# Kernel optimization log

Hardware: AMD Instinct MI355X
Metric: run time of the kernel (lower is better)

Reference implementation:

```python
import jax, jax.numpy as jnp
import numpy as np

B, N, D, H, DH = 2, 4096, 256, 8, 64   # batch, nodes, dim, heads, dim_head
INNER = H * DH
POLY_K = 3  # polynomial order -> coeffs [H, POLY_K+1]
LN_EPS = 1e-5


def setup_inputs() -> dict:
    key = jax.random.key(0)
    ks = jax.random.split(key, 8)
    s = 0.02
    return {
        "x": jax.random.normal(ks[0], (B, N, D), dtype=jnp.float32),
        "Wq": jax.random.normal(ks[1], (D, INNER), dtype=jnp.float32) * s,
        "Wk": jax.random.normal(ks[2], (D, INNER), dtype=jnp.float32) * s,
        "Wv": jax.random.normal(ks[3], (D, INNER), dtype=jnp.float32) * s,
        "Wo": jax.random.normal(ks[4], (INNER, D), dtype=jnp.float32) * s,
        "gamma": jnp.ones((DH,), dtype=jnp.float32),
        "beta": jnp.zeros((DH,), dtype=jnp.float32),
        "coeffs": jax.random.normal(ks[5], (H, POLY_K + 1), dtype=jnp.float32) * 0.5,
    }


def reference(x, Wq, Wk, Wv, Wo, gamma, beta, coeffs):
    b, n, d = x.shape
    h, dh = coeffs.shape[0], gamma.shape[0]
    # --- graph estimator: per-head softmax adjacency A = softmax(QK^T/sqrt(dh)) ---
    q = (x @ Wq).reshape(b, n, h, dh).transpose(0, 2, 1, 3)  # bhnd
    k = (x @ Wk).reshape(b, n, h, dh).transpose(0, 2, 1, 3)  # bhnd
    scale = jax.lax.rsqrt(jnp.asarray(dh, x.dtype))
    A = jax.nn.softmax(jnp.einsum('bhnd,bhmd->bhnm', q, k) * scale, axis=-1)
    # --- value projection + per-head LayerNorm over dim_head ---
    v = (x @ Wv).reshape(b, n, h, dh)
    mu = v.mean(axis=-1, keepdims=True)
    var = ((v - mu) ** 2).mean(axis=-1, keepdims=True)
    v = (v - mu) * jax.lax.rsqrt(var + LN_EPS) * gamma + beta
    v = v.transpose(0, 2, 1, 3)  # bhnd
    # --- polynomial graph filter: y = sum_k c[h,k] * A^k v ---
    y = coeffs[None, :, 0, None, None] * v
    t = v
    for kk in range(1, coeffs.shape[1]):
        t = jnp.einsum('bhnm,bhmd->bhnd', A, t)
        y = y + coeffs[None, :, kk, None, None] * t
    # --- merge heads + output projection ---
    merged = y.transpose(0, 2, 1, 3).reshape(b, n, h * dh)
    return merged @ Wo
```

## Files before the change

kernel.cpp:

```cpp
#include <hip/hip_runtime.h>
#include <stdint.h>

#define B_ 2
#define N_ 4096
#define D_ 256
#define H_ 8
#define DH_ 64
#define INNER_ 512
#define NBH 16
#define PAD 72
#define FPAD 80

typedef unsigned short ushort_t;
typedef __attribute__((ext_vector_type(8))) short short8;
typedef __attribute__((ext_vector_type(4))) float float4v;
typedef __attribute__((ext_vector_type(4))) unsigned short ushort4v;
typedef __attribute__((ext_vector_type(4))) unsigned int uint4v;

__device__ __forceinline__ ushort_t f2bf(float f) {
    union { float f; unsigned int u; } v; v.f = f;
    unsigned int r = v.u + 0x7FFFu + ((v.u >> 16) & 1u);
    return (ushort_t)(r >> 16);
}
__device__ __forceinline__ float bf2f(ushort_t u) {
    union { unsigned int u; float f; } v; v.u = ((unsigned int)u) << 16;
    return v.f;
}
__device__ __forceinline__ unsigned char f2fp8s(float f) {
    union { float f; unsigned int u; } v; v.f = f;
    unsigned int s = (v.u >> 24) & 0x80u;
    v.u &= 0x7FFFFFFFu;
    float a = v.f;
    if (a >= 448.f) return (unsigned char)(s | 0x7E);
    if (a < 0.015625f) {
        int m = (int)(a * 512.f + 0.5f);
        return (unsigned char)(s | (unsigned)m);
    }
    unsigned int u = v.u + 0x7FFFFu + ((v.u >> 20) & 1u);
    return (unsigned char)(s | (((u >> 20) & 0x7FF) - 960));
}
__device__ __forceinline__ float fexp2(float x) {
    float r;
    asm volatile("v_exp_f32 %0, %1\n\ts_nop 0" : "=v"(r) : "v"(x));
    return r;
}

__global__ __launch_bounds__(256) void prep_kernel(
    const float* __restrict__ x, const float* __restrict__ Wq,
    const float* __restrict__ Wk, const float* __restrict__ Wv,
    const float* __restrict__ Wo,
    ushort_t* __restrict__ xb, ushort_t* __restrict__ WqkvT,
    ushort_t* __restrict__ WoT) {
    int idx = blockIdx.x * 256 + threadIdx.x;
    const int total_x = B_ * N_ * D_;
    const int total_wqkv = 3 * INNER_ * D_;
    const int total_wo = D_ * INNER_;
    if (idx < total_x) { xb[idx] = f2bf(x[idx]); return; }
    idx -= total_x;
    if (idx < total_wqkv) {
        int n = idx >> 8, k = idx & 255;
        int which = n >> 9, nn = n & 511;
        const float* W = (which == 0) ? Wq : ((which == 1) ? Wk : Wv);
        WqkvT[idx] = f2bf(W[k * INNER_ + nn]);
        return;
    }
    idx -= total_wqkv;
    if (idx < total_wo) {
        int c = idx >> 9, k = idx & 511;
        WoT[idx] = f2bf(Wo[k * D_ + c]);
    }
}

__global__ __launch_bounds__(256) void proj_gemm(
    const ushort_t* __restrict__ xb, const ushort_t* __restrict__ WqkvT,
    ushort_t* __restrict__ Qb, ushort_t* __restrict__ Kb,
    ushort_t* __restrict__ Vb) {
    __shared__ ushort_t As[128][PAD];
    __shared__ ushort_t Bs[128][PAD];
    int bid = blockIdx.x;
    int tileN = bid % 12, tileM = bid / 12;
    int tid = threadIdx.x;
    int w = tid >> 6, lane = tid & 63, q = lane >> 4, r = lane & 15;
    int wr = (w & 1) * 64, wc = (w >> 1) * 64;
    float4v acc[4][4];
    for (int i = 0; i < 4; i++)
        for (int j = 0; j < 4; j++)
            for (int e = 0; e < 4; e++) acc[i][j][e] = 0.f;

    for (int k0 = 0; k0 < 256; k0 += 64) {
        for (int it = 0; it < 4; it++) {
            int idx = tid + it * 256;
            int row = idx >> 3, kc = (idx & 7) * 8;
            *(short8*)&As[row][kc] =
                *(const short8*)&xb[(size_t)(tileM * 128 + row) * 256 + k0 + kc];
            *(short8*)&Bs[row][kc] =
                *(const short8*)&WqkvT[(size_t)(tileN * 128 + row) * 256 + k0 + kc];
        }
        __syncthreads();
        for (int kk = 0; kk < 64; kk += 32) {
            short8 a[4], b[4];
            for (int mi = 0; mi < 4; mi++)
                a[mi] = *(const short8*)&As[wr + mi * 16 + r][kk + q * 8];
            for (int ni = 0; ni < 4; ni++)
                b[ni] = *(const short8*)&Bs[wc + ni * 16 + r][kk + q * 8];
            for (int mi = 0; mi < 4; mi++)
                for (int ni = 0; ni < 4; ni++)
                    acc[mi][ni] = __builtin_amdgcn_mfma_f32_16x16x32_bf16(
                        a[mi], b[ni], acc[mi][ni], 0, 0, 0);
        }
        __syncthreads();
    }
    for (int mi = 0; mi < 4; mi++)
        for (int ni = 0; ni < 4; ni++)
            for (int reg = 0; reg < 4; reg++) {
                int grow = tileM * 128 + wr + mi * 16 + q * 4 + reg;
                int gcol = tileN * 128 + wc + ni * 16 + r;
                float v = acc[mi][ni][reg];
                int which = gcol >> 9, inner = gcol & 511;
                int h = inner >> 6, d = inner & 63;
                int b = grow >> 12, n = grow & 4095;
                size_t off = (((size_t)(b * H_ + h)) * N_ + n) * DH_ + d;
                if (which == 0) Qb[off] = f2bf(v * 0.18033688011112042f);
                else if (which == 1) Kb[off] = f2bf(v);
                else Vb[off] = f2bf(v);
            }
}

__global__ __launch_bounds__(256) void ln_kernel(
    const ushort_t* __restrict__ Vb, const float* __restrict__ gamma,
    const float* __restrict__ beta, const float* __restrict__ coeffs,
    unsigned char* __restrict__ t0T, float* __restrict__ y) {
    int tid = threadIdx.x;
    int wave = tid >> 6, lane = tid & 63;
    size_t row = (size_t)blockIdx.x * 4 + wave;
    int bh = (int)(row >> 12), n = (int)(row & 4095);
    int h = bh & 7;
    float v = bf2f(Vb[row * 64 + lane]);
    float s = v;
    for (int m = 32; m >= 1; m >>= 1) s += __shfl_xor(s, m, 64);
    float mu = s * (1.f / 64.f);
    float dv = v - mu;
    float s2 = dv * dv;
    for (int m = 32; m >= 1; m >>= 1) s2 += __shfl_xor(s2, m, 64);
    float var = s2 * (1.f / 64.f);
    float vln = dv * rsqrtf(var + 1e-5f) * gamma[lane] + beta[lane];
    float c0 = coeffs[h * 4 + 0];
    y[row * 64 + lane] = c0 * vln;
    t0T[((size_t)bh * 64 + lane) * 4096 + n] = f2fp8s(vln);
}


#define MFB(a, b, c) __builtin_amdgcn_mfma_f32_16x16x32_bf16(a, b, c, 0, 0, 0)
#define MFP(a, b, c) __builtin_amdgcn_mfma_f32_16x16x32_fp8_fp8(a, b, c, 0, 0, 0)

__device__ __forceinline__ long pk8(float4v x, float4v y) {
    int d0 = __builtin_amdgcn_cvt_pk_fp8_f32(fexp2(x[0]), fexp2(x[1]), 0, false);
    d0 = __builtin_amdgcn_cvt_pk_fp8_f32(fexp2(x[2]), fexp2(x[3]), d0, true);
    int d1 = __builtin_amdgcn_cvt_pk_fp8_f32(fexp2(y[0]), fexp2(y[1]), 0, false);
    d1 = __builtin_amdgcn_cvt_pk_fp8_f32(fexp2(y[2]), fexp2(y[3]), d1, true);
    return (long)(((unsigned long)(unsigned int)d1 << 32) | (unsigned int)d0);
}

#define WGBAR()                                                \
    do {                                                       \
        asm volatile("s_waitcnt lgkmcnt(0)" ::: "memory");     \
        __builtin_amdgcn_sched_barrier(0);                     \
        __builtin_amdgcn_s_barrier();                          \
        __builtin_amdgcn_sched_barrier(0);                     \
    } while (0)

#define COMPUTE32(KsX, TsX)                                                     \
    {                                                                           \
        short8 a0, a1;                                                          \
        float4v s00, s10, s20, s30, s01, s11, s21, s31;                         \
        a0 = *(const short8*)&KsX[r][q * 8];                                    \
        a1 = *(const short8*)&KsX[r][32 + q * 8];                               \
        s00 = MFB(a1, qf1, MFB(a0, qf0, zf));                                   \
        s01 = MFB(a1, qf3, MFB(a0, qf2, zf));                                   \
        a0 = *(const short8*)&KsX[16 + r][q * 8];                               \
        a1 = *(const short8*)&KsX[16 + r][32 + q * 8];                          \
        s10 = MFB(a1, qf1, MFB(a0, qf0, zf));                                   \
        s11 = MFB(a1, qf3, MFB(a0, qf2, zf));                                   \
        a0 = *(const short8*)&KsX[32 + r][q * 8];                               \
        a1 = *(const short8*)&KsX[32 + r][32 + q * 8];                          \
        s20 = MFB(a1, qf1, MFB(a0, qf0, zf));                                   \
        s21 = MFB(a1, qf3, MFB(a0, qf2, zf));                                   \
        a0 = *(const short8*)&KsX[48 + r][q * 8];                               \
        a1 = *(const short8*)&KsX[48 + r][32 + q * 8];                          \
        s30 = MFB(a1, qf1, MFB(a0, qf0, zf));                                   \
        s31 = MFB(a1, qf3, MFB(a0, qf2, zf));                                   \
        long eA0 = pk8(s00, s10), eB0 = pk8(s20, s30);                          \
        long eA1 = pk8(s01, s11), eB1 = pk8(s21, s31);                          \
        long b0 = *(const long*)&TsX[r][q * 8];                                 \
        long b1 = *(const long*)&TsX[16 + r][q * 8];                            \
        long b2 = *(const long*)&TsX[32 + r][q * 8];                            \
        long b3 = *(const long*)&TsX[48 + r][q * 8];                            \
        acc0[0] = MFP(eA0, b0, acc0[0]); acc1[0] = MFP(eA1, b0, acc1[0]);       \
        acc0[1] = MFP(eA0, b1, acc0[1]); acc1[1] = MFP(eA1, b1, acc1[1]);       \
        acc0[2] = MFP(eA0, b2, acc0[2]); acc1[2] = MFP(eA1, b2, acc1[2]);       \
        acc0[3] = MFP(eA0, b3, acc0[3]); acc1[3] = MFP(eA1, b3, acc1[3]);       \
        accs0 = MFP(eA0, bones, accs0);  accs1 = MFP(eA1, bones, accs1);        \
        b0 = *(const long*)&TsX[r][32 + q * 8];                                 \
        b1 = *(const long*)&TsX[16 + r][32 + q * 8];                            \
        b2 = *(const long*)&TsX[32 + r][32 + q * 8];                            \
        b3 = *(const long*)&TsX[48 + r][32 + q * 8];                            \
        acc0[0] = MFP(eB0, b0, acc0[0]); acc1[0] = MFP(eB1, b0, acc1[0]);       \
        acc0[1] = MFP(eB0, b1, acc0[1]); acc1[1] = MFP(eB1, b1, acc1[1]);       \
        acc0[2] = MFP(eB0, b2, acc0[2]); acc1[2] = MFP(eB1, b2, acc1[2]);       \
        acc0[3] = MFP(eB0, b3, acc0[3]); acc1[3] = MFP(eB1, b3, acc1[3]);       \
        accs0 = MFP(eB0, bones, accs0);  accs1 = MFP(eB1, bones, accs1);        \
    }

__global__ __launch_bounds__(256) void poly_pass(
    const ushort_t* __restrict__ Qb, const ushort_t* __restrict__ Kb,
    const unsigned char* __restrict__ tinT, float* __restrict__ y,
    unsigned char* __restrict__ toutT, const float* __restrict__ coeffs,
    int kidx, int write_t) {
    __shared__ ushort_t Ks0[64][PAD];
    __shared__ ushort_t Ks1[64][PAD];
    __shared__ unsigned char Ts0[64][FPAD];
    __shared__ unsigned char Ts1[64][FPAD];
    int bid0 = blockIdx.x;
    int bid = ((bid0 & 7) << 6) | (bid0 >> 3);
    int bh = bid >> 5, ti = bid & 31;
    const ushort_t* Q = Qb + (size_t)bh * N_ * 64;
    const ushort_t* K = Kb + (size_t)bh * N_ * 64;
    const unsigned char* tin = tinT + (size_t)bh * 64 * N_;
    int tid = threadIdx.x, w = tid >> 6, lane = tid & 63, q = lane >> 4, r = lane & 15;
    const float4v zf = {0.f, 0.f, 0.f, 0.f};

    const ushort_t* qp = Q + (size_t)(ti * 128 + w * 32 + r) * 64 + q * 8;
    short8 qf0 = *(const short8*)qp;
    short8 qf1 = *(const short8*)(qp + 32);
    short8 qf2 = *(const short8*)(qp + 16 * 64);
    short8 qf3 = *(const short8*)(qp + 16 * 64 + 32);

    float4v acc0[4], acc1[4], accs0, accs1;
    for (int e = 0; e < 4; e++) { accs0[e] = 0.f; accs1[e] = 0.f; }
    for (int j = 0; j < 4; j++)
        for (int e = 0; e < 4; e++) { acc0[j][e] = 0.f; acc1[j][e] = 0.f; }
    const long bones = 0x3838383838383838L;

    int krow = tid >> 2, kpart = (tid & 3) * 16;
    int Lrow = (krow & 32) + ((krow & 4) << 2) + (krow & 3) + ((krow >> 3) & 3) * 4;
    const ushort_t* kp = K + (size_t)krow * 64 + kpart;
    int srow = tid >> 2, scol = (tid & 3) * 16;
    const unsigned char* tp = tin + (size_t)srow * 4096 + scol;

    {
        uint4v ka = *(const uint4v*)kp;
        uint4v kb = *(const uint4v*)(kp + 8);
        uint4v tv = *(const uint4v*)tp;
        *(uint4v*)&Ks0[Lrow][kpart] = ka;
        *(uint4v*)&Ks0[Lrow][kpart + 8] = kb;
        *(uint4v*)&Ts0[srow][scol] = tv;
    }
    uint4v pka = *(const uint4v*)(kp + 4096);
    uint4v pkb = *(const uint4v*)(kp + 4096 + 8);
    uint4v pt  = *(const uint4v*)(tp + 64);
    const ushort_t* kpl = kp + 2 * 4096;
    const unsigned char* tpl = tp + 2 * 64;
    WGBAR();

    for (int it = 0; it < 64; it += 2) {
        *(uint4v*)&Ks1[Lrow][kpart] = pka;
        *(uint4v*)&Ks1[Lrow][kpart + 8] = pkb;
        *(uint4v*)&Ts1[srow][scol] = pt;
        pka = *(const uint4v*)kpl;
        pkb = *(const uint4v*)(kpl + 8);
        pt  = *(const uint4v*)tpl;
        kpl += 4096; tpl += 64;
        COMPUTE32(Ks0, Ts0);
        WGBAR();
        *(uint4v*)&Ks0[Lrow][kpart] = pka;
        *(uint4v*)&Ks0[Lrow][kpart + 8] = pkb;
        *(uint4v*)&Ts0[srow][scol] = pt;
        pka = *(const uint4v*)kpl;
        pkb = *(const uint4v*)(kpl + 8);
        pt  = *(const uint4v*)tpl;
        kpl += 4096; tpl += 64;
        COMPUTE32(Ks1, Ts1);
        WGBAR();
    }

    int h = bh & 7;
    float ck = coeffs[h * 4 + kidx];
    float rinv0[4], rinv1[4];
#pragma unroll
    for (int reg = 0; reg < 4; reg++) {
        rinv0[reg] = 1.f / accs0[reg];
        rinv1[reg] = 1.f / accs1[reg];
    }
    float tv0[4][4], tv1[4][4];
#pragma unroll
    for (int ni = 0; ni < 4; ni++)
#pragma unroll
        for (int reg = 0; reg < 4; reg++) {
            tv0[ni][reg] = acc0[ni][reg] * rinv0[reg];
            tv1[ni][reg] = acc1[ni][reg] * rinv1[reg];
        }
#pragma unroll
    for (int reg = 0; reg < 4; reg++) {
        int il = w * 32 + q * 4 + reg;
        float* yp0 = y + ((size_t)bh * N_ + (size_t)ti * 128 + il) * 64;
        float* yp1 = yp0 + 16 * 64;
#pragma unroll
        for (int ni = 0; ni < 4; ni++) {
            yp0[ni * 16 + r] += ck * tv0[ni][reg];
            yp1[ni * 16 + r] += ck * tv1[ni][reg];
        }
    }
    if (write_t) {
        unsigned char (*TT)[144] = (unsigned char(*)[144])&Ks0[0][0];
#pragma unroll
        for (int ni = 0; ni < 4; ni++) {
            int p0 = __builtin_amdgcn_cvt_pk_fp8_f32(tv0[ni][0], tv0[ni][1], 0, false);
            p0 = __builtin_amdgcn_cvt_pk_fp8_f32(tv0[ni][2], tv0[ni][3], p0, true);
            *(unsigned int*)&TT[ni * 16 + r][w * 32 + q * 4] = (unsigned int)p0;
            int p1 = __builtin_amdgcn_cvt_pk_fp8_f32(tv1[ni][0], tv1[ni][1], 0, false);
            p1 = __builtin_amdgcn_cvt_pk_fp8_f32(tv1[ni][2], tv1[ni][3], p1, true);
            *(unsigned int*)&TT[ni * 16 + r][w * 32 + 16 + q * 4] = (unsigned int)p1;
        }
        WGBAR();
        int drow = tid >> 2, dcol = (tid & 3) * 32;
        uint4v v0 = *(const uint4v*)&TT[drow][dcol];
        uint4v v1 = *(const uint4v*)&TT[drow][dcol + 16];
        unsigned char* dst =
            toutT + (size_t)bh * 64 * N_ + (size_t)drow * N_ + ti * 128 + dcol;
        *(uint4v*)dst = v0;
        *(uint4v*)(dst + 16) = v1;
    }
}

__global__ __launch_bounds__(256) void out_gemm(
    const float* __restrict__ y, const ushort_t* __restrict__ WoT,
    float* __restrict__ out) {
    __shared__ ushort_t As[128][PAD];
    __shared__ ushort_t Bs[64][PAD];
    int bid = blockIdx.x;
    int tileN = bid & 3, tileM = bid >> 2;
    int tid = threadIdx.x, w = tid >> 6, lane = tid & 63, q = lane >> 4, r = lane & 15;
    int wr = w * 32;
    float4v acc[2][4];
    for (int i = 0; i < 2; i++)
        for (int j = 0; j < 4; j++)
            for (int e = 0; e < 4; e++) acc[i][j][e] = 0.f;

    for (int k0 = 0; k0 < 512; k0 += 64) {
        int h = k0 >> 6;
        for (int it = 0; it < 8; it++) {
            int idx = tid + it * 256;
            int row = idx >> 4, kc = (idx & 15) * 4;
            int grow = tileM * 128 + row;
            int b = grow >> 12, n = grow & 4095;
            const float4* src =
                (const float4*)&y[(((size_t)(b * H_ + h)) * N_ + n) * 64 + kc];
            float4 v = *src;
            ushort4v pv;
            pv[0] = f2bf(v.x); pv[1] = f2bf(v.y); pv[2] = f2bf(v.z); pv[3] = f2bf(v.w);
            *(ushort4v*)&As[row][kc] = pv;
        }
        for (int it = 0; it < 2; it++) {
            int idx = tid + it * 256;
            int row = idx >> 3, kc = (idx & 7) * 8;
            *(short8*)&Bs[row][kc] =
                *(const short8*)&WoT[(size_t)(tileN * 64 + row) * 512 + k0 + kc];
        }
        __syncthreads();
        for (int kk = 0; kk < 64; kk += 32) {
            short8 a[2], b[4];
            a[0] = *(const short8*)&As[wr + r][kk + q * 8];
            a[1] = *(const short8*)&As[wr + 16 + r][kk + q * 8];
            for (int ni = 0; ni < 4; ni++)
                b[ni] = *(const short8*)&Bs[ni * 16 + r][kk + q * 8];
            for (int mi = 0; mi < 2; mi++)
                for (int ni = 0; ni < 4; ni++)
                    acc[mi][ni] = __builtin_amdgcn_mfma_f32_16x16x32_bf16(
                        a[mi], b[ni], acc[mi][ni], 0, 0, 0);
        }
        __syncthreads();
    }
    for (int mi = 0; mi < 2; mi++)
        for (int reg = 0; reg < 4; reg++) {
            int grow = tileM * 128 + wr + mi * 16 + q * 4 + reg;
            for (int ni = 0; ni < 4; ni++) {
                int gcol = tileN * 64 + ni * 16 + r;
                out[(size_t)grow * 256 + gcol] = acc[mi][ni][reg];
            }
        }
}

extern "C" void kernel_launch(void* const* d_in, const int* in_sizes, int n_in,
                              void* d_out, int out_size, void* d_ws, size_t ws_size,
                              hipStream_t stream) {
    const float* x      = (const float*)d_in[0];
    const float* Wq     = (const float*)d_in[1];
    const float* Wk     = (const float*)d_in[2];
    const float* Wv     = (const float*)d_in[3];
    const float* Wo     = (const float*)d_in[4];
    const float* gamma  = (const float*)d_in[5];
    const float* beta   = (const float*)d_in[6];
    const float* coeffs = (const float*)d_in[7];
    float* out = (float*)d_out;

    char* ws = (char*)d_ws;
    size_t off = 0;
    auto alloc = [&](size_t bytes) -> void* {
        void* p = ws + off;
        off += (bytes + 255) & ~(size_t)255;
        return p;
    };
    ushort_t* xb    = (ushort_t*)alloc((size_t)B_ * N_ * D_ * 2);
    ushort_t* WqkvT = (ushort_t*)alloc((size_t)3 * INNER_ * D_ * 2);
    ushort_t* WoT   = (ushort_t*)alloc((size_t)D_ * INNER_ * 2);
    ushort_t* Qb    = (ushort_t*)alloc((size_t)NBH * N_ * DH_ * 2);
    ushort_t* Kb    = (ushort_t*)alloc((size_t)NBH * N_ * DH_ * 2);
    ushort_t* Vb    = (ushort_t*)alloc((size_t)NBH * N_ * DH_ * 2);
    unsigned char* t0T = (unsigned char*)alloc((size_t)NBH * DH_ * N_);
    unsigned char* t1T = (unsigned char*)alloc((size_t)NBH * DH_ * N_);
    float*    y     = (float*)alloc((size_t)NBH * N_ * DH_ * 4);

    const int prep_total = B_ * N_ * D_ + 3 * INNER_ * D_ + D_ * INNER_;
    prep_kernel<<<(prep_total + 255) / 256, 256, 0, stream>>>(
        x, Wq, Wk, Wv, Wo, xb, WqkvT, WoT);
    proj_gemm<<<768, 256, 0, stream>>>(xb, WqkvT, Qb, Kb, Vb);
    ln_kernel<<<(NBH * N_) / 4, 256, 0, stream>>>(Vb, gamma, beta, coeffs, t0T, y);

    poly_pass<<<NBH * 32, 256, 0, stream>>>(Qb, Kb, t0T, y, t1T, coeffs, 1, 1);
    poly_pass<<<NBH * 32, 256, 0, stream>>>(Qb, Kb, t1T, y, t0T, coeffs, 2, 1);
    poly_pass<<<NBH * 32, 256, 0, stream>>>(Qb, Kb, t0T, y, t1T, coeffs, 3, 0);

    out_gemm<<<256, 256, 0, stream>>>(y, WoT, out);
}
```

Before: 391.7 us.

## Split poly_pass key dimension across two wave groups with LDS reduction

Each poly_pass block now runs 512 threads, with two groups of four waves each processing half of the key/node range (2048 keys each) for the same 128 query rows. Each half keeps its own double-buffered K and T tiles in a shared 56KB LDS buffer. After the loop, the second half writes its partial accumulators to LDS and the first half sums them before normalization, the y update and the fp8 transpose write. The aim is to raise parallelism and latency hiding with only 512 blocks on the device, at the cost of more LDS per block, an extra reduction barrier and idle waves in the epilogue.

```diff
diff --git a/kernel.cpp b/kernel.cpp
--- a/kernel.cpp
+++ b/kernel.cpp
@@ -211,15 +211,19 @@
         accs0 = MFP(eB0, bones, accs0);  accs1 = MFP(eB1, bones, accs1);        \
     }
 
-__global__ __launch_bounds__(256) void poly_pass(
+__global__ __launch_bounds__(512, 4) void poly_pass(
     const ushort_t* __restrict__ Qb, const ushort_t* __restrict__ Kb,
     const unsigned char* __restrict__ tinT, float* __restrict__ y,
     unsigned char* __restrict__ toutT, const float* __restrict__ coeffs,
     int kidx, int write_t) {
-    __shared__ ushort_t Ks0[64][PAD];
-    __shared__ ushort_t Ks1[64][PAD];
-    __shared__ unsigned char Ts0[64][FPAD];
-    __shared__ unsigned char Ts1[64][FPAD];
+    __shared__ char smem[57344];
+    typedef ushort_t KsArr[64][PAD];
+    typedef unsigned char TsArr[64][FPAD];
+    KsArr* Ks0 = (KsArr*)smem;
+    KsArr* Ks1 = (KsArr*)(smem + 18432);
+    TsArr* Ts0 = (TsArr*)(smem + 36864);
+    TsArr* Ts1 = (TsArr*)(smem + 47104);
+
     int bid0 = blockIdx.x;
     int bid = ((bid0 & 7) << 6) | (bid0 >> 3);
     int bh = bid >> 5, ti = bid & 31;
@@ -227,9 +231,10 @@
     const ushort_t* K = Kb + (size_t)bh * N_ * 64;
     const unsigned char* tin = tinT + (size_t)bh * 64 * N_;
     int tid = threadIdx.x, w = tid >> 6, lane = tid & 63, q = lane >> 4, r = lane & 15;
+    int half = w >> 2, wsub = w & 3;
     const float4v zf = {0.f, 0.f, 0.f, 0.f};
 
-    const ushort_t* qp = Q + (size_t)(ti * 128 + w * 32 + r) * 64 + q * 8;
+    const ushort_t* qp = Q + (size_t)(ti * 128 + wsub * 32 + r) * 64 + q * 8;
     short8 qf0 = *(const short8*)qp;
     short8 qf1 = *(const short8*)(qp + 32);
     short8 qf2 = *(const short8*)(qp + 16 * 64);
@@ -241,19 +246,20 @@
         for (int e = 0; e < 4; e++) { acc0[j][e] = 0.f; acc1[j][e] = 0.f; }
     const long bones = 0x3838383838383838L;
 
-    int krow = tid >> 2, kpart = (tid & 3) * 16;
+    int tl = tid & 255;
+    int krow = tl >> 2, kpart = (tl & 3) * 16;
     int Lrow = (krow & 32) + ((krow & 4) << 2) + (krow & 3) + ((krow >> 3) & 3) * 4;
-    const ushort_t* kp = K + (size_t)krow * 64 + kpart;
-    int srow = tid >> 2, scol = (tid & 3) * 16;
-    const unsigned char* tp = tin + (size_t)srow * 4096 + scol;
+    const ushort_t* kp = K + (size_t)(half * 2048 + krow) * 64 + kpart;
+    int srow = tl >> 2, scol = (tl & 3) * 16;
+    const unsigned char* tp = tin + (size_t)srow * 4096 + half * 2048 + scol;
 
     {
         uint4v ka = *(const uint4v*)kp;
         uint4v kb = *(const uint4v*)(kp + 8);
         uint4v tv = *(const uint4v*)tp;
-        *(uint4v*)&Ks0[Lrow][kpart] = ka;
-        *(uint4v*)&Ks0[Lrow][kpart + 8] = kb;
-        *(uint4v*)&Ts0[srow][scol] = tv;
+        *(uint4v*)&Ks0[half][Lrow][kpart] = ka;
+        *(uint4v*)&Ks0[half][Lrow][kpart + 8] = kb;
+        *(uint4v*)&Ts0[half][srow][scol] = tv;
     }
     uint4v pka = *(const uint4v*)(kp + 4096);
     uint4v pkb = *(const uint4v*)(kp + 4096 + 8);
@@ -262,73 +268,95 @@
     const unsigned char* tpl = tp + 2 * 64;
     WGBAR();
 
-    for (int it = 0; it < 64; it += 2) {
-        *(uint4v*)&Ks1[Lrow][kpart] = pka;
-        *(uint4v*)&Ks1[Lrow][kpart + 8] = pkb;
-        *(uint4v*)&Ts1[srow][scol] = pt;
+    for (int it = 0; it < 32; it += 2) {
+        *(uint4v*)&Ks1[half][Lrow][kpart] = pka;
+        *(uint4v*)&Ks1[half][Lrow][kpart + 8] = pkb;
+        *(uint4v*)&Ts1[half][srow][scol] = pt;
         pka = *(const uint4v*)kpl;
         pkb = *(const uint4v*)(kpl + 8);
         pt  = *(const uint4v*)tpl;
         kpl += 4096; tpl += 64;
-        COMPUTE32(Ks0, Ts0);
+        COMPUTE32(Ks0[half], Ts0[half]);
         WGBAR();
-        *(uint4v*)&Ks0[Lrow][kpart] = pka;
-        *(uint4v*)&Ks0[Lrow][kpart + 8] = pkb;
-        *(uint4v*)&Ts0[srow][scol] = pt;
+        *(uint4v*)&Ks0[half][Lrow][kpart] = pka;
+        *(uint4v*)&Ks0[half][Lrow][kpart + 8] = pkb;
+        *(uint4v*)&Ts0[half][srow][scol] = pt;
         pka = *(const uint4v*)kpl;
         pkb = *(const uint4v*)(kpl + 8);
         pt  = *(const uint4v*)tpl;
         kpl += 4096; tpl += 64;
-        COMPUTE32(Ks1, Ts1);
+        COMPUTE32(Ks1[half], Ts1[half]);
         WGBAR();
     }
 
-    int h = bh & 7;
-    float ck = coeffs[h * 4 + kidx];
-    float rinv0[4], rinv1[4];
-#pragma unroll
-    for (int reg = 0; reg < 4; reg++) {
-        rinv0[reg] = 1.f / accs0[reg];
-        rinv1[reg] = 1.f / accs1[reg];
-    }
-    float tv0[4][4], tv1[4][4];
-#pragma unroll
-    for (int ni = 0; ni < 4; ni++)
+    float* ULDS = (float*)smem;
+    unsigned char (*TT)[144] = (unsigned char(*)[144])(smem + 40960);
+
+    if (half == 1) {
+        float* ub = ULDS + (size_t)(wsub * 64 + lane) * 40;
+#pragma unroll
+        for (int j = 0; j < 4; j++) {
+            *(float4v*)(ub + j * 4) = acc0[j];
+            *(float4v*)(ub + 16 + j * 4) = acc1[j];
+        }
+        *(float4v*)(ub + 32) = accs0;
+        *(float4v*)(ub + 36) = accs1;
+    }
+    WGBAR();
+    if (half == 0) {
+        const float* ub = ULDS + (size_t)(wsub * 64 + lane) * 40;
+#pragma unroll
+        for (int j = 0; j < 4; j++) {
+            acc0[j] += *(const float4v*)(ub + j * 4);
+            acc1[j] += *(const float4v*)(ub + 16 + j * 4);
+        }
+        accs0 += *(const float4v*)(ub + 32);
+        accs1 += *(const float4v*)(ub + 36);
+
+        int h = bh & 7;
+        float ck = coeffs[h * 4 + kidx];
+        float rinv0[4], rinv1[4];
 #pragma unroll
         for (int reg = 0; reg < 4; reg++) {
-            tv0[ni][reg] = acc0[ni][reg] * rinv0[reg];
-            tv1[ni][reg] = acc1[ni][reg] * rinv1[reg];
-        }
-#pragma unroll
-    for (int reg = 0; reg < 4; reg++) {
-        int il = w * 32 + q * 4 + reg;
-        float* yp0 = y + ((size_t)bh * N_ + (size_t)ti * 128 + il) * 64;
-        float* yp1 = yp0 + 16 * 64;
-#pragma unroll
-        for (int ni = 0; ni < 4; ni++) {
-            yp0[ni * 16 + r] += ck * tv0[ni][reg];
-            yp1[ni * 16 + r] += ck * tv1[ni][reg];
+            rinv0[reg] = 1.f / accs0[reg];
+            rinv1[reg] = 1.f / accs1[reg];
+        }
+        float tv0[4][4], tv1[4][4];
+#pragma unroll
+        for (int ni = 0; ni < 4; ni++)
+#pragma unroll
+            for (int reg = 0; reg < 4; reg++) {
+                tv0[ni][reg] = acc0[ni][reg] * rinv0[reg];
+                tv1[ni][reg] = acc1[ni][reg] * rinv1[reg];
+            }
+#pragma unroll
+        for (int reg = 0; reg < 4; reg++) {
+            int il = wsub * 32 + q * 4 + reg;
+            float* yp0 = y + ((size_t)bh * N_ + (size_t)ti * 128 + il) * 64;
+            float* yp1 = yp0 + 16 * 64;
+#pragma unroll
+            for (int ni = 0; ni < 4; ni++) {
+                yp0[ni * 16 + r] += ck * tv0[ni][reg];
+                yp1[ni * 16 + r] += ck * tv1[ni][reg];
+            }
+        }
+        if (write_t) {
+#pragma unroll
+            for (int ni = 0; ni < 4; ni++) {
+                int p0 = __builtin_amdgcn_cvt_pk_fp8_f32(tv0[ni][0], tv0[ni][1], 0, false);
+                p0 = __builtin_amdgcn_cvt_pk_fp8_f32(tv0[ni][2], tv0[ni][3], p0, true);
+                *(unsigned int*)&TT[ni * 16 + r][wsub * 32 + q * 4] = (unsigned int)p0;
+                int p1 = __builtin_amdgcn_cvt_pk_fp8_f32(tv1[ni][0], tv1[ni][1], 0, false);
+                p1 = __builtin_amdgcn_cvt_pk_fp8_f32(tv1[ni][2], tv1[ni][3], p1, true);
+                *(unsigned int*)&TT[ni * 16 + r][wsub * 32 + 16 + q * 4] = (unsigned int)p1;
+            }
         }
     }
     if (write_t) {
-        unsigned char (*TT)[144] = (unsigned char(*)[144])&Ks0[0][0];
-#pragma unroll
-        for (int ni = 0; ni < 4; ni++) {
-            int p0 = __builtin_amdgcn_cvt_pk_fp8_f32(tv0[ni][0], tv0[ni][1], 0, false);
-            p0 = __builtin_amdgcn_cvt_pk_fp8_f32(tv0[ni][2], tv0[ni][3], p0, true);
-            *(unsigned int*)&TT[ni * 16 + r][w * 32 + q * 4] = (unsigned int)p0;
-            int p1 = __builtin_amdgcn_cvt_pk_fp8_f32(tv1[ni][0], tv1[ni][1], 0, false);
-            p1 = __builtin_amdgcn_cvt_pk_fp8_f32(tv1[ni][2], tv1[ni][3], p1, true);
-            *(unsigned int*)&TT[ni * 16 + r][w * 32 + 16 + q * 4] = (unsigned int)p1;
-        }
         WGBAR();
-        int drow = tid >> 2, dcol = (tid & 3) * 32;
-        uint4v v0 = *(const uint4v*)&TT[drow][dcol];
-        uint4v v1 = *(const uint4v*)&TT[drow][dcol + 16];
-        unsigned char* dst =
-            toutT + (size_t)bh * 64 * N_ + (size_t)drow * N_ + ti * 128 + dcol;
-        *(uint4v*)dst = v0;
-        *(uint4v*)(dst + 16) = v1;
+        int drow = tid >> 3, dcol = (tid & 7) * 16;
+        uint4v vv = *(const uint4v*)&TT[drow][dcol];
+        *(uint4v*)&toutT[(size_t)bh * 64 * N_ + (size_t)drow * N_ + ti * 128 + dcol] = vv;
     }
 }
 
@@ -426,9 +454,9 @@
     proj_gemm<<<768, 256, 0, stream>>>(xb, WqkvT, Qb, Kb, Vb);
     ln_kernel<<<(NBH * N_) / 4, 256, 0, stream>>>(Vb, gamma, beta, coeffs, t0T, y);
 
-    poly_pass<<<NBH * 32, 256, 0, stream>>>(Qb, Kb, t0T, y, t1T, coeffs, 1, 1);
-    poly_pass<<<NBH * 32, 256, 0, stream>>>(Qb, Kb, t1T, y, t0T, coeffs, 2, 1);
-    poly_pass<<<NBH * 32, 256, 0, stream>>>(Qb, Kb, t0T, y, t1T, coeffs, 3, 0);
+    poly_pass<<<NBH * 32, 512, 0, stream>>>(Qb, Kb, t0T, y, t1T, coeffs, 1, 1);
+    poly_pass<<<NBH * 32, 512, 0, stream>>>(Qb, Kb, t1T, y, t0T, coeffs, 2, 1);
+    poly_pass<<<NBH * 32, 512, 0, stream>>>(Qb, Kb, t0T, y, t1T, coeffs, 3, 0);
 
     out_gemm<<<256, 256, 0, stream>>>(y, WoT, out);
 }
```

Measured after the change: 361.2 us. 1.08x faster.
